# Kernel tuning notes

Hardware: AMD Instinct MI355X
Metric: run time of the kernel (lower is better)

Reference implementation:

```python
import jax, jax.numpy as jnp
import numpy as np
import math

LN_EPS = 1e-5
EPS = 1e-8

def _unfold3(x, stride):
    # torch nn.Unfold(kernel_size=3, stride=stride, padding=1); output [B, C*9, L]
    B, C, H, W = x.shape
    xp = jnp.pad(x, ((0, 0), (0, 0), (1, 1), (1, 1)))
    Ho = (H + 2 - 3) // stride + 1
    Wo = (W + 2 - 3) // stride + 1
    pats = [xp[:, :, i:i + stride * (Ho - 1) + 1:stride, j:j + stride * (Wo - 1) + 1:stride]
            for i in range(3) for j in range(3)]
    out = jnp.stack(pats, axis=2)  # [B,C,9,Ho,Wo]  (c-major, then kh,kw: torch ordering)
    return out.reshape(B, C * 9, Ho * Wo)

def _ln(x, g, b):
    mu = jnp.mean(x, axis=-1, keepdims=True)
    var = jnp.mean((x - mu) ** 2, axis=-1, keepdims=True)
    return (x - mu) * jax.lax.rsqrt(var + LN_EPS) * g + b

def _prm_exp(x, w):
    # x: [B,T,emb], w: [m,emb] -> [B,T,m]
    m = w.shape[0]
    xd = jnp.sum(x * x, axis=-1, keepdims=True) / 2.0
    wtx = jnp.einsum('bte,me->btm', x, w)
    return jnp.exp(wtx - xd) / math.sqrt(m)

def _performer(x, kqv_w, kqv_b, pw, pb, g1, b1, g2, b2, m1w, m1b, m2w, m2b, w):
    # Token_performer.forward (dropout = identity, eval mode)
    h = _ln(x, g1, b1)
    kqv = h @ kqv_w.T + kqv_b
    k, q, v = jnp.split(kqv, 3, axis=-1)  # torch.split order: k, q, v
    kp = _prm_exp(k, w)
    qp = _prm_exp(q, w)
    D = jnp.einsum('btm,bm->bt', qp, kp.sum(axis=1))[..., None]        # [B,T,1]
    kptv = jnp.einsum('btn,btm->bnm', v, kp)                            # [B,emb,m]
    y = jnp.einsum('btm,bnm->btn', qp, kptv) / (D + EPS)                # [B,T,emb]
    y = v + (y @ pw.T + pb)
    h2 = _ln(y, g2, b2)
    mlp = jax.nn.gelu(h2 @ m1w.T + m1b, approximate=False) @ m2w.T + m2b
    return y + mlp

def _forward(x,
             p1_kqv_w, p1_kqv_b, p1_proj_w, p1_proj_b, p1_n1_g, p1_n1_b, p1_n2_g, p1_n2_b,
             p1_m1_w, p1_m1_b, p1_m2_w, p1_m2_b, p1_w,
             p2_kqv_w, p2_kqv_b, p2_proj_w, p2_proj_b, p2_n1_g, p2_n1_b, p2_n2_g, p2_n2_b,
             p2_m1_w, p2_m1_b, p2_m2_w, p2_m2_b, p2_w,
             proj_w, proj_b):
    t = _unfold3(x, 1).transpose(0, 2, 1)  # [B, 50176, 27]
    t = _performer(t, p1_kqv_w, p1_kqv_b, p1_proj_w, p1_proj_b, p1_n1_g, p1_n1_b,
                   p1_n2_g, p1_n2_b, p1_m1_w, p1_m1_b, p1_m2_w, p1_m2_b, p1_w)
    B, N, C = t.shape
    s = int(math.isqrt(N))
    t = t.transpose(0, 2, 1).reshape(B, C, s, s)
    t = _unfold3(t, 2).transpose(0, 2, 1)  # [B, 12544, 576]
    t = _performer(t, p2_kqv_w, p2_kqv_b, p2_proj_w, p2_proj_b, p2_n1_g, p2_n1_b,
                   p2_n2_g, p2_n2_b, p2_m1_w, p2_m1_b, p2_m2_w, p2_m2_b, p2_w)
    B, N, C = t.shape
    s = int(math.isqrt(N))
    t = t.transpose(0, 2, 1).reshape(B, C, s, s)
    t = _unfold3(t, 2).transpose(0, 2, 1)  # [B, 3136, 576]
    return t @ proj_w.T + proj_b           # [B, 3136, 768]

def setup_inputs() -> dict:
    key = jax.random.key(0)
    ks = iter(jax.random.split(key, 40))
    def rn(shape, scale=0.02):
        return (jax.random.normal(next(ks), shape, dtype=jnp.float32) * scale)
    EMB, M = 64, 32
    inp = {'x': jax.random.normal(next(ks), (8, 3, 224, 224), dtype=jnp.float32)}
    for pfx, dim in (('p1', 27), ('p2', 576)):
        inp[f'{pfx}_kqv_w'] = rn((3 * EMB, dim))
        inp[f'{pfx}_kqv_b'] = jnp.zeros((3 * EMB,), jnp.float32)
        inp[f'{pfx}_proj_w'] = rn((EMB, EMB))
        inp[f'{pfx}_proj_b'] = jnp.zeros((EMB,), jnp.float32)
        inp[f'{pfx}_n1_g'] = jnp.ones((dim,), jnp.float32)
        inp[f'{pfx}_n1_b'] = jnp.zeros((dim,), jnp.float32)
        inp[f'{pfx}_n2_g'] = jnp.ones((EMB,), jnp.float32)
        inp[f'{pfx}_n2_b'] = jnp.zeros((EMB,), jnp.float32)
        inp[f'{pfx}_m1_w'] = rn((EMB, EMB))
        inp[f'{pfx}_m1_b'] = jnp.zeros((EMB,), jnp.float32)
        inp[f'{pfx}_m2_w'] = rn((EMB, EMB))
        inp[f'{pfx}_m2_b'] = jnp.zeros((EMB,), jnp.float32)
        # frozen random-feature projection, scaled ~ orthogonal * sqrt(m)
        inp[f'{pfx}_w'] = jax.random.normal(next(ks), (M, EMB), dtype=jnp.float32)
    inp['proj_w'] = rn((768, 576))
    inp['proj_b'] = jnp.zeros((768,), jnp.float32)
    return inp

def reference(x,
              p1_kqv_w, p1_kqv_b, p1_proj_w, p1_proj_b, p1_n1_g, p1_n1_b, p1_n2_g, p1_n2_b,
              p1_m1_w, p1_m1_b, p1_m2_w, p1_m2_b, p1_w,
              p2_kqv_w, p2_kqv_b, p2_proj_w, p2_proj_b, p2_n1_g, p2_n1_b, p2_n2_g, p2_n2_b,
              p2_m1_w, p2_m1_b, p2_m2_w, p2_m2_b, p2_w,
              proj_w, proj_b):
    return _forward(x,
                    p1_kqv_w, p1_kqv_b, p1_proj_w, p1_proj_b, p1_n1_g, p1_n1_b, p1_n2_g, p1_n2_b,
                    p1_m1_w, p1_m1_b, p1_m2_w, p1_m2_b, p1_w,
                    p2_kqv_w, p2_kqv_b, p2_proj_w, p2_proj_b, p2_n1_g, p2_n1_b, p2_n2_g, p2_n2_b,
                    p2_m1_w, p2_m1_b, p2_m2_w, p2_m2_b, p2_w,
                    proj_w, proj_b)
```

## Files before the change

### kernel.cpp

```cpp
#include <hip/hip_runtime.h>
#include <hip/hip_bf16.h>
#include <math.h>

typedef __hip_bfloat16 bf16;
typedef __attribute__((ext_vector_type(8))) short frag8;
typedef __attribute__((ext_vector_type(4))) float f32x4;
typedef long long ll;

__device__ __forceinline__ float b2f(bf16 v) { return __bfloat162float(v); }
__device__ __forceinline__ bf16 f2b(float v) { return __float2bfloat16(v); }

__device__ __forceinline__ unsigned pk2f(float a, float b) {
    union { bf16 h[2]; unsigned u; } c;
    c.h[0] = f2b(a); c.h[1] = f2b(b);
    return c.u;
}
__device__ __forceinline__ void up8(const bf16* p, float* f) {
    const uint4 u = *(const uint4*)p;
    union { unsigned u; bf16 h[2]; } c;
    c.u = u.x; f[0] = b2f(c.h[0]); f[1] = b2f(c.h[1]);
    c.u = u.y; f[2] = b2f(c.h[0]); f[3] = b2f(c.h[1]);
    c.u = u.z; f[4] = b2f(c.h[0]); f[5] = b2f(c.h[1]);
    c.u = u.w; f[6] = b2f(c.h[0]); f[7] = b2f(c.h[1]);
}
__device__ __forceinline__ void up8u(const uint4 u, float* f) {
    union { unsigned u; bf16 h[2]; } c;
    c.u = u.x; f[0] = b2f(c.h[0]); f[1] = b2f(c.h[1]);
    c.u = u.y; f[2] = b2f(c.h[0]); f[3] = b2f(c.h[1]);
    c.u = u.z; f[4] = b2f(c.h[0]); f[5] = b2f(c.h[1]);
    c.u = u.w; f[6] = b2f(c.h[0]); f[7] = b2f(c.h[1]);
}

#define LN_EPS 1e-5f
#define D_EPS 1e-8f
#define INV_SQRT_M 0.17677669529663687f

__global__ __launch_bounds__(256) void k_sniff(const void* x, int* mode)
{
    __shared__ int cnt;
    if (threadIdx.x == 0) cnt = 0;
    __syncthreads();
    const unsigned short* u = (const unsigned short*)x;
    const unsigned short h = u[2 * threadIdx.x];
    const unsigned int bits = ((unsigned int)h) << 16;
    const float v = __uint_as_float(bits);
    const float a = fabsf(v);
    const bool sane = (h == 0) || (a >= 1e-8f && a <= 1e4f);
    if (!sane) atomicAdd(&cnt, 1);
    __syncthreads();
    if (threadIdx.x == 0) *mode = (cnt > 64) ? 1 : 0;
}

struct CvTab { const void* src[28]; int dstOff[28]; int cum[29]; };

__global__ __launch_bounds__(256) void k_convert_all(CvTab tab, bf16* base,
                                                     const int* mode)
{
    const int idx = blockIdx.x * 256 + threadIdx.x;
    if (idx >= tab.cum[28]) return;
    int s = 0;
    while (idx >= tab.cum[s + 1]) ++s;
    const int local = idx - tab.cum[s];
    const float v = (*mode) ? ((const float*)tab.src[s])[local]
                            : b2f(((const bf16*)tab.src[s])[local]);
    base[tab.dstOff[s] + local] = f2b(v);
}

__global__ __launch_bounds__(256) void k_prep(
    const void* __restrict__ w1raw, const int* __restrict__ mode,
    bf16* __restrict__ w1ph, bf16* __restrict__ w1pl)
{
    const int idx = blockIdx.x * 256 + threadIdx.x;
    if (idx >= 6144) return;
    const int o = idx >> 5, k = idx & 31;
    float v = 0.f;
    if (k < 27)
        v = (*mode) ? ((const float*)w1raw)[o * 27 + k]
                    : b2f(((const bf16*)w1raw)[o * 27 + k]);
    const bf16 h = f2b(v);
    w1ph[idx] = h;
    w1pl[idx] = f2b(v - b2f(h));
}

__global__ __launch_bounds__(256) void k_fused1(
    const bf16* __restrict__ x, const bf16* __restrict__ w1ph,
    const bf16* __restrict__ w1pl, const bf16* __restrict__ kqvb,
    const bf16* __restrict__ n1g, const bf16* __restrict__ n1b,
    const bf16* __restrict__ pw,
    bf16* __restrict__ KP, bf16* __restrict__ QP, bf16* __restrict__ V,
    float* __restrict__ red, const int b)
{
    __shared__ __align__(16) char smem[49632];
    bf16 (*wps)[72] = (bf16(*)[72])(smem);
    bf16 (*Ah)[40]  = (bf16(*)[40])(smem + 4608);
    bf16 (*Al)[40]  = (bf16(*)[40])(smem + 9728);
    bf16 (*Th)[72]  = (bf16(*)[72])(smem + 14848);
    bf16 (*Tl)[72]  = (bf16(*)[72])(smem + 24064);
    bf16 (*Wh)[40]  = (bf16(*)[40])(smem + 33280);
    bf16 (*Wl)[40]  = (bf16(*)[40])(smem + 38400);
    bf16 (*KPs)[40] = (bf16(*)[40])(smem + 43520);
    bf16 (*Vs)[72]  = (bf16(*)[72])(smem + 14848);
    float* kbs = (float*)(smem + 48640);
    float* gs  = (float*)(smem + 49408);
    float* bs  = (float*)(smem + 49520);

    const int tid = threadIdx.x;
    {
        const int i = tid * 8;
        *(uint4*)(&wps[i >> 6][i & 63]) = *(const uint4*)(pw + i);
    }
    if (tid < 192) kbs[tid] = b2f(kqvb[tid]);
    if (tid < 27) { gs[tid] = b2f(n1g[tid]); bs[tid] = b2f(n1b[tid]); }
    if (blockIdx.x == 0)
        for (int i = tid; i < 2080; i += 256) red[i] = 0.f;

    const int tok = tid >> 2, part = tid & 3;
    const int t = blockIdx.x * 64 + tok;
    const int h = t / 224, w = t - h * 224;
    const int d0 = part * 7;
    const int nd = (part == 3) ? 6 : 7;
    float vals[7];
    float s = 0.f;
    #pragma unroll
    for (int q = 0; q < 7; ++q) {
        float val = 0.f;
        if (q < nd) {
            const int d = d0 + q;
            const int c = d / 9, rr = d - c * 9;
            const int pi = rr / 3, pj = rr - pi * 3;
            const int hh = h + pi - 1, ww = w + pj - 1;
            if (hh >= 0 && hh < 224 && ww >= 0 && ww < 224)
                val = b2f(x[((ll)(b * 3 + c) * 224 + hh) * 224 + ww]);
        }
        vals[q] = val; s += val;
    }
    s += __shfl_xor(s, 1, 64);  s += __shfl_xor(s, 2, 64);
    const float mean = s * (1.f / 27.f);
    float s2 = 0.f;
    #pragma unroll
    for (int q = 0; q < 7; ++q) {
        if (q < nd) { const float dd = vals[q] - mean; s2 += dd * dd; }
    }
    s2 += __shfl_xor(s2, 1, 64); s2 += __shfl_xor(s2, 2, 64);
    const float rs = rsqrtf(s2 * (1.f / 27.f) + LN_EPS);
    __syncthreads();
    #pragma unroll
    for (int q = 0; q < 7; ++q) {
        if (q < nd) {
            const int d = d0 + q;
            const float nv = (vals[q] - mean) * rs * gs[d] + bs[d];
            const bf16 nh = f2b(nv);
            Ah[tok][d] = nh;
            Al[tok][d] = f2b(nv - b2f(nh));
        }
    }
    if (part == 3) {
        #pragma unroll
        for (int d = 27; d < 32; ++d) { Ah[tok][d] = f2b(0.f); Al[tok][d] = f2b(0.f); }
    }

    const int wv = tid >> 6, lane = tid & 63;
    const int l15 = lane & 15;
    const int k8 = (lane >> 4) << 3;
    const int rbase = (lane >> 4) << 2;
    const int srow = tid >> 2;
    const int scol = (tid & 3) << 3;
    const int colg = (tid & 3) << 4;

    float xdK[4], xdQ[4];

    #pragma unroll
    for (int g = 0; g < 3; ++g) {
        *(uint4*)(&Wh[srow][scol]) = *(const uint4*)(w1ph + (g * 64 + srow) * 32 + scol);
        *(uint4*)(&Wl[srow][scol]) = *(const uint4*)(w1pl + (g * 64 + srow) * 32 + scol);
        __syncthreads();
        const frag8 ah = *(const frag8*)(&Ah[(wv << 4) + l15][k8]);
        const frag8 al = *(const frag8*)(&Al[(wv << 4) + l15][k8]);
        f32x4 acc[4] = {};
        #pragma unroll
        for (int nt = 0; nt < 4; ++nt) {
            const frag8 bh = *(const frag8*)(&Wh[(nt << 4) + l15][k8]);
            const frag8 bl = *(const frag8*)(&Wl[(nt << 4) + l15][k8]);
            acc[nt] = __builtin_amdgcn_mfma_f32_16x16x32_bf16(ah, bh, acc[nt], 0, 0, 0);
            acc[nt] = __builtin_amdgcn_mfma_f32_16x16x32_bf16(al, bh, acc[nt], 0, 0, 0);
            acc[nt] = __builtin_amdgcn_mfma_f32_16x16x32_bf16(ah, bl, acc[nt], 0, 0, 0);
            acc[nt] = __builtin_amdgcn_mfma_f32_16x16x32_bf16(al, bl, acc[nt], 0, 0, 0);
        }
        float xdp[4] = {0.f, 0.f, 0.f, 0.f};
        #pragma unroll
        for (int nt = 0; nt < 4; ++nt) {
            const int col = (nt << 4) + l15;
            const float bv = kbs[g * 64 + col];
            #pragma unroll
            for (int r = 0; r < 4; ++r) {
                const float tb = acc[nt][r] + bv;
                const int trow = (wv << 4) + rbase + r;
                if (g < 2) {
                    const bf16 th = f2b(tb);
                    Th[trow][col] = th;
                    Tl[trow][col] = f2b(tb - b2f(th));
                    xdp[r] += tb * tb;
                } else {
                    Vs[trow][col] = f2b(tb);
                }
            }
        }
        if (g < 2) {
            #pragma unroll
            for (int r = 0; r < 4; ++r) {
                float v = xdp[r];
                v += __shfl_xor(v, 1, 64); v += __shfl_xor(v, 2, 64);
                v += __shfl_xor(v, 4, 64); v += __shfl_xor(v, 8, 64);
                if (g == 0) xdK[r] = 0.5f * v; else xdQ[r] = 0.5f * v;
            }
        }
        __syncthreads();
        if (g < 2) {
            f32x4 acc2[2] = {};
            #pragma unroll
            for (int k0 = 0; k0 < 64; k0 += 32) {
                const frag8 ath = *(const frag8*)(&Th[(wv << 4) + l15][k8 + k0]);
                const frag8 atl = *(const frag8*)(&Tl[(wv << 4) + l15][k8 + k0]);
                #pragma unroll
                for (int nt = 0; nt < 2; ++nt) {
                    const frag8 bw = *(const frag8*)(&wps[(nt << 4) + l15][k8 + k0]);
                    acc2[nt] = __builtin_amdgcn_mfma_f32_16x16x32_bf16(ath, bw, acc2[nt], 0, 0, 0);
                    acc2[nt] = __builtin_amdgcn_mfma_f32_16x16x32_bf16(atl, bw, acc2[nt], 0, 0, 0);
                }
            }
            #pragma unroll
            for (int nt = 0; nt < 2; ++nt)
                #pragma unroll
                for (int r = 0; r < 4; ++r) {
                    const float xd = (g == 0) ? xdK[r] : xdQ[r];
                    const float p = expf(fminf(acc2[nt][r] - xd, 30.f)) * INV_SQRT_M;
                    KPs[(wv << 4) + rbase + r][(nt << 4) + l15] = f2b(p);
                }
            __syncthreads();
            bf16* dstP = (g == 0 ? KP : QP) + ((ll)blockIdx.x * 64 + srow) * 32 + scol;
            *(uint4*)dstP = *(const uint4*)(&KPs[srow][scol]);
            __syncthreads();
        } else {
            bf16* dstV = V + ((ll)blockIdx.x * 64 + srow) * 64 + colg;
            *(uint4*)dstV       = *(const uint4*)(&Vs[srow][colg]);
            *(uint4*)(dstV + 8) = *(const uint4*)(&Vs[srow][colg + 8]);
        }
    }
}

__global__ __launch_bounds__(256) void k_reduce(
    const bf16* __restrict__ kpB, const bf16* __restrict__ vB, const int vstride,
    const int T, float* __restrict__ redBase, const int chunk)
{
    __shared__ bf16 VT[64][72];
    __shared__ bf16 KT[32][72];
    const int bz = blockIdx.y;
    const bf16* kp = kpB + (ll)bz * T * 32;
    const bf16* v  = vB + (ll)bz * T * (ll)vstride;
    float* red = redBase + (ll)bz * 2080;
    const int tid = threadIdx.x;
    const int wv = tid >> 6, lane = tid & 63;
    const int l15 = lane & 15, k8 = (lane >> 4) << 3, rbase = (lane >> 4) << 2;
    const int t0 = blockIdx.x * chunk;

    frag8 ones;
    {
        union { bf16 h; short s; } u; u.h = f2b(1.f);
        #pragma unroll
        for (int i = 0; i < 8; ++i) ones[i] = u.s;
    }

    f32x4 acc[2] = {};
    f32x4 accK[2] = {};

    for (int tt = 0; tt < chunk; tt += 64) {
        const int tb = t0 + tt;
        __syncthreads();
        {
            const int tk = tid >> 2, n0 = (tid & 3) << 4;
            const bf16* src = v + (ll)(tb + tk) * vstride + n0;
            bf16 tmp[16];
            *(uint4*)tmp       = *(const uint4*)src;
            *(uint4*)(tmp + 8) = *(const uint4*)(src + 8);
            #pragma unroll
            for (int j = 0; j < 16; ++j) VT[n0 + j][tk] = tmp[j];
        }
        {
            const int tk = tid >> 2, m0 = (tid & 3) << 3;
            const bf16* src = kp + (ll)(tb + tk) * 32 + m0;
            bf16 tmp[8];
            *(uint4*)tmp = *(const uint4*)src;
            #pragma unroll
            for (int j = 0; j < 8; ++j) KT[m0 + j][tk] = tmp[j];
        }
        __syncthreads();
        #pragma unroll
        for (int ks = 0; ks < 2; ++ks) {
            const frag8 af = *(const frag8*)(&VT[(wv << 4) + l15][k8 + ks * 32]);
            #pragma unroll
            for (int tn = 0; tn < 2; ++tn) {
                const frag8 bfv = *(const frag8*)(&KT[(tn << 4) + l15][k8 + ks * 32]);
                acc[tn] = __builtin_amdgcn_mfma_f32_16x16x32_bf16(af, bfv, acc[tn], 0, 0, 0);
            }
            if (wv == 0) {
                #pragma unroll
                for (int tn = 0; tn < 2; ++tn) {
                    const frag8 bfv = *(const frag8*)(&KT[(tn << 4) + l15][k8 + ks * 32]);
                    accK[tn] = __builtin_amdgcn_mfma_f32_16x16x32_bf16(ones, bfv, accK[tn], 0, 0, 0);
                }
            }
        }
    }
    #pragma unroll
    for (int tn = 0; tn < 2; ++tn) {
        const int m = (tn << 4) + l15;
        #pragma unroll
        for (int r = 0; r < 4; ++r) {
            const int n = (wv << 4) + rbase + r;
            atomicAdd(&red[n * 32 + m], acc[tn][r]);
        }
    }
    if (wv == 0 && (lane >> 4) == 0) {
        #pragma unroll
        for (int tn = 0; tn < 2; ++tn)
            atomicAdd(&red[2048 + (tn << 4) + l15], accK[tn][0]);
    }
}

__global__ __launch_bounds__(256) void k_postmlp(
    const bf16* __restrict__ qpB, const float* __restrict__ redBase,
    const bf16* __restrict__ vB, const int vstride,
    const bf16* __restrict__ pw, const bf16* __restrict__ pb,
    const bf16* __restrict__ n2g, const bf16* __restrict__ n2b,
    const bf16* __restrict__ w1, const bf16* __restrict__ b1,
    const bf16* __restrict__ w2, const bf16* __restrict__ b2,
    bf16* outB, const int T)
{
    __shared__ __align__(16) char smem[47232];
    bf16 (*QPs)[40] = (bf16(*)[40])(smem);
    bf16 (*KH)[40]  = (bf16(*)[40])(smem + 5120);
    bf16 (*KL)[40]  = (bf16(*)[40])(smem + 10240);
    float (*Cs)[72] = (float(*)[72])(smem);
    bf16 (*W1s)[72] = (bf16(*)[72])(smem);
    bf16 (*W2s)[72] = (bf16(*)[72])(smem + 9216);
    bf16 (*PWs)[72] = (bf16(*)[72])(smem + 18432);
    bf16 (*Gs)[72]  = (bf16(*)[72])(smem + 18432);
    bf16 (*Y0H)[72] = (bf16(*)[72])(smem + 27648);
    bf16 (*Ys)[72]  = (bf16(*)[72])(smem + 27648);
    bf16 (*Y0L)[72] = (bf16(*)[72])(smem + 36864);
    bf16 (*Hn)[72]  = (bf16(*)[72])(smem + 36864);
    float* invs  = (float*)(smem + 46080);
    float* pbs   = (float*)(smem + 46336);
    float* ksums = (float*)(smem + 46592);
    float* mns   = (float*)(smem + 46720);
    float* rss   = (float*)(smem + 46976);

    const int tid = threadIdx.x;
    const int bz = blockIdx.y;
    const float* red = redBase + (ll)bz * 2080;
    const bf16* qp = qpB + (ll)bz * (ll)T * 32;
    const bf16* v  = vB + (ll)bz * (ll)T * (ll)vstride;
    bf16* out = outB + (ll)bz * (ll)T * 64;
    const ll m0 = (ll)blockIdx.x * 64;

    const int lr = tid >> 2;
    const int lc8 = (tid & 3) << 3;
    const int lc16 = (tid & 3) << 4;

    *(uint4*)(&QPs[lr][lc8]) = *(const uint4*)(qp + (m0 + lr) * 32 + lc8);
    *(uint4*)(&PWs[lr][lc16])     = *(const uint4*)(pw + lr * 64 + lc16);
    *(uint4*)(&PWs[lr][lc16 + 8]) = *(const uint4*)(pw + lr * 64 + lc16 + 8);
    {
        const int i0 = tid * 8;
        const float4 a = *(const float4*)(red + i0);
        const float4 b = *(const float4*)(red + i0 + 4);
        const int n = i0 >> 5, m = i0 & 31;
        float xs[8] = {a.x, a.y, a.z, a.w, b.x, b.y, b.z, b.w};
        #pragma unroll
        for (int k = 0; k < 8; ++k) {
            const bf16 h = f2b(xs[k]);
            KH[n][m + k] = h;
            KL[n][m + k] = f2b(xs[k] - b2f(h));
        }
    }
    if (tid < 32) ksums[tid] = red[2048 + tid];
    if (tid < 64) pbs[tid] = b2f(pb[tid]);
    __syncthreads();

    if (tid < 64) {
        float D = D_EPS;
        #pragma unroll
        for (int m = 0; m < 32; ++m) D += b2f(QPs[tid][m]) * ksums[m];
        invs[tid] = 1.f / D;
    }

    const int wv = tid >> 6, lane = tid & 63;
    const int l15 = lane & 15;
    const int mr = (wv << 4) + l15;
    const int k8 = (lane >> 4) << 3;
    const int rbase = (lane >> 4) << 2;

    f32x4 acc[4] = {};
    {
        const frag8 af = *(const frag8*)(&QPs[mr][k8]);
        #pragma unroll
        for (int tn = 0; tn < 4; ++tn) {
            const int nr = (tn << 4) + l15;
            const frag8 bh = *(const frag8*)(&KH[nr][k8]);
            acc[tn] = __builtin_amdgcn_mfma_f32_16x16x32_bf16(af, bh, acc[tn], 0, 0, 0);
            const frag8 bl = *(const frag8*)(&KL[nr][k8]);
            acc[tn] = __builtin_amdgcn_mfma_f32_16x16x32_bf16(af, bl, acc[tn], 0, 0, 0);
        }
    }
    #pragma unroll
    for (int tn = 0; tn < 4; ++tn) {
        const int n = (tn << 4) + l15;
        #pragma unroll
        for (int r = 0; r < 4; ++r) {
            const float x = acc[tn][r];
            const bf16 h = f2b(x);
            Y0H[(wv << 4) + rbase + r][n] = h;
            Y0L[(wv << 4) + rbase + r][n] = f2b(x - b2f(h));
        }
    }
    __syncthreads();

    f32x4 acc2[4] = {};
    #pragma unroll
    for (int k0 = 0; k0 < 64; k0 += 32) {
        const frag8 ah = *(const frag8*)(&Y0H[mr][k8 + k0]);
        const frag8 al = *(const frag8*)(&Y0L[mr][k8 + k0]);
        #pragma unroll
        for (int tn = 0; tn < 4; ++tn) {
            const frag8 bw = *(const frag8*)(&PWs[(tn << 4) + l15][k8 + k0]);
            acc2[tn] = __builtin_amdgcn_mfma_f32_16x16x32_bf16(ah, bw, acc2[tn], 0, 0, 0);
            acc2[tn] = __builtin_amdgcn_mfma_f32_16x16x32_bf16(al, bw, acc2[tn], 0, 0, 0);
        }
    }
    #pragma unroll
    for (int tn = 0; tn < 4; ++tn) {
        const int n = (tn << 4) + l15;
        #pragma unroll
        for (int r = 0; r < 4; ++r) {
            const int row = (wv << 4) + rbase + r;
            Cs[row][n] = acc2[tn][r] * invs[row] + pbs[n];
        }
    }
    __syncthreads();

    {
        const int row = tid >> 2;
        const bf16* vsrc = v + (m0 + row) * (ll)vstride + lc16;
        #pragma unroll
        for (int hh = 0; hh < 2; ++hh) {
            float vv[8];
            up8(vsrc + hh * 8, vv);
            const float* cp = &Cs[row][lc16 + hh * 8];
            uint4 st;
            st.x = pk2f(cp[0] + vv[0], cp[1] + vv[1]);
            st.y = pk2f(cp[2] + vv[2], cp[3] + vv[3]);
            st.z = pk2f(cp[4] + vv[4], cp[5] + vv[5]);
            st.w = pk2f(cp[6] + vv[6], cp[7] + vv[7]);
            *(uint4*)(&Ys[row][lc16 + hh * 8]) = st;
        }
    }
    __syncthreads();

    if (tid < 64) {
        float s = 0.f, s2 = 0.f;
        #pragma unroll
        for (int n = 0; n < 64; ++n) { const float vv = b2f(Ys[tid][n]); s += vv; s2 += vv * vv; }
        const float mn = s * (1.f / 64.f);
        const float var = fmaxf(s2 * (1.f / 64.f) - mn * mn, 0.f);
        mns[tid] = mn; rss[tid] = rsqrtf(var + LN_EPS);
    }
    *(uint4*)(&W1s[lr][lc16])     = *(const uint4*)(w1 + lr * 64 + lc16);
    *(uint4*)(&W1s[lr][lc16 + 8]) = *(const uint4*)(w1 + lr * 64 + lc16 + 8);
    *(uint4*)(&W2s[lr][lc16])     = *(const uint4*)(w2 + lr * 64 + lc16);
    *(uint4*)(&W2s[lr][lc16 + 8]) = *(const uint4*)(w2 + lr * 64 + lc16 + 8);
    __syncthreads();

    for (int i = tid; i < 4096; i += 256) {
        const int r = i >> 6, c = i & 63;
        Hn[r][c] = f2b((b2f(Ys[r][c]) - mns[r]) * rss[r] * b2f(n2g[c]) + b2f(n2b[c]));
    }
    __syncthreads();

    f32x4 accm[4] = {};
    #pragma unroll
    for (int k0 = 0; k0 < 64; k0 += 32) {
        const frag8 af = *(const frag8*)(&Hn[mr][k8 + k0]);
        #pragma unroll
        for (int tn = 0; tn < 4; ++tn) {
            const frag8 bfv = *(const frag8*)(&W1s[(tn << 4) + l15][k8 + k0]);
            accm[tn] = __builtin_amdgcn_mfma_f32_16x16x32_bf16(af, bfv, accm[tn], 0, 0, 0);
        }
    }
    #pragma unroll
    for (int tn = 0; tn < 4; ++tn) {
        const int n = (tn << 4) + l15;
        const float bv = b2f(b1[n]);
        #pragma unroll
        for (int r = 0; r < 4; ++r) {
            float vg = accm[tn][r] + bv;
            vg = 0.5f * vg * (1.f + erff(vg * 0.70710678118654752f));
            Gs[(wv << 4) + rbase + r][n] = f2b(vg);
        }
    }
    __syncthreads();

    f32x4 accn[4] = {};
    #pragma unroll
    for (int k0 = 0; k0 < 64; k0 += 32) {
        const frag8 af = *(const frag8*)(&Gs[mr][k8 + k0]);
        #pragma unroll
        for (int tn = 0; tn < 4; ++tn) {
            const frag8 bfv = *(const frag8*)(&W2s[(tn << 4) + l15][k8 + k0]);
            accn[tn] = __builtin_amdgcn_mfma_f32_16x16x32_bf16(af, bfv, accn[tn], 0, 0, 0);
        }
    }
    #pragma unroll
    for (int tn = 0; tn < 4; ++tn) {
        const int n = (tn << 4) + l15;
        const float bv = b2f(b2[n]);
        #pragma unroll
        for (int r = 0; r < 4; ++r)
            Hn[(wv << 4) + rbase + r][n] = f2b(accn[tn][r] + bv);
    }
    __syncthreads();

    {
        const int row = tid >> 2;
        bf16* dst = out + (m0 + row) * 64 + lc16;
        #pragma unroll
        for (int hh = 0; hh < 2; ++hh) {
            float sv[8], rv[8];
            up8(&Hn[row][lc16 + hh * 8], sv);
            up8(&Ys[row][lc16 + hh * 8], rv);
            uint4 st;
            st.x = pk2f(sv[0] + rv[0], sv[1] + rv[1]);
            st.y = pk2f(sv[2] + rv[2], sv[3] + rv[3]);
            st.z = pk2f(sv[4] + rv[4], sv[5] + rv[5]);
            st.w = pk2f(sv[6] + rv[6], sv[7] + rv[7]);
            *(uint4*)(dst + hh * 8) = st;
        }
    }
}

__global__ __launch_bounds__(256) void k_unfold576(
    const bf16* __restrict__ in, const int Hin, const int Ho,
    const bf16* __restrict__ g, const bf16* __restrict__ bb,
    const int do_ln, bf16* __restrict__ A,
    const ll inBStride, const ll outBStride)
{
    in += (ll)blockIdx.y * inBStride;
    A  += (ll)blockIdx.y * outBStride;
    const int t = blockIdx.x * 4 + (threadIdx.x >> 6);
    const int l = threadIdx.x & 63;
    const int ho = t / Ho, wo = t - ho * Ho;
    float vals[9];
    float s = 0.f;
    #pragma unroll
    for (int r = 0; r < 9; ++r) {
        const int d = l + (r << 6);
        const int c = d / 9;
        const int rr = d - c * 9;
        const int i = rr / 3, j = rr - i * 3;
        const int hh = 2 * ho + i - 1, ww = 2 * wo + j - 1;
        float val = 0.f;
        if (hh >= 0 && hh < Hin && ww >= 0 && ww < Hin)
            val = b2f(in[((ll)hh * Hin + ww) * 64 + c]);
        vals[r] = val; s += val;
    }
    bf16* out = A + (ll)t * 576;
    if (do_ln) {
        #pragma unroll
        for (int o = 32; o > 0; o >>= 1) s += __shfl_xor(s, o, 64);
        const float mean = s * (1.f / 576.f);
        float s2 = 0.f;
        #pragma unroll
        for (int r = 0; r < 9; ++r) { const float dd = vals[r] - mean; s2 += dd * dd; }
        #pragma unroll
        for (int o = 32; o > 0; o >>= 1) s2 += __shfl_xor(s2, o, 64);
        const float rs = rsqrtf(s2 * (1.f / 576.f) + LN_EPS);
        #pragma unroll
        for (int r = 0; r < 9; ++r) {
            const int d = l + (r << 6);
            out[d] = f2b((vals[r] - mean) * rs * b2f(g[d]) + b2f(bb[d]));
        }
    } else {
        #pragma unroll
        for (int r = 0; r < 9; ++r) out[l + (r << 6)] = f2b(vals[r]);
    }
}

__global__ __launch_bounds__(256) void k_gemm(
    const bf16* __restrict__ A, const int lda,
    const bf16* __restrict__ W,
    const bf16* __restrict__ bias,
    const bf16* res, const int ldres,
    void* C, const int ldc, const ll mOff,
    const int K, const int* outm)
{
    __shared__ bf16 As[2][64][40];
    __shared__ bf16 Bs[2][64][40];
    __shared__ bf16 Cs[64][72];
    const int tid = threadIdx.x;
    const int wv = tid >> 6;
    const int lane = tid & 63;
    const ll m0 = (ll)blockIdx.x * 64;
    const int n0 = blockIdx.y * 64;
    f32x4 acc[4] = {};
    const int lr = tid >> 2;
    const int lc = (tid & 3) << 3;
    const int mr = (wv << 4) + (lane & 15);
    const int k8 = (lane >> 4) << 3;
    const bf16* Ag = A + (m0 + lr) * (ll)lda + lc;
    const bf16* Wg = W + (ll)(n0 + lr) * K + lc;

    uint4 av  = *(const uint4*)(Ag);
    uint4 wv4 = *(const uint4*)(Wg);
    *(uint4*)(&As[0][lr][lc]) = av;
    *(uint4*)(&Bs[0][lr][lc]) = wv4;
    int cur = 0;
    __syncthreads();
    for (int k0 = 0; k0 < K; k0 += 32) {
        const bool nxt = (k0 + 32 < K);
        if (nxt) {
            av  = *(const uint4*)(Ag + k0 + 32);
            wv4 = *(const uint4*)(Wg + k0 + 32);
        }
        const frag8 af = *(const frag8*)(&As[cur][mr][k8]);
        #pragma unroll
        for (int tn = 0; tn < 4; ++tn) {
            const frag8 bfv = *(const frag8*)(&Bs[cur][(tn << 4) + (lane & 15)][k8]);
            acc[tn] = __builtin_amdgcn_mfma_f32_16x16x32_bf16(af, bfv, acc[tn], 0, 0, 0);
        }
        if (nxt) {
            *(uint4*)(&As[cur ^ 1][lr][lc]) = av;
            *(uint4*)(&Bs[cur ^ 1][lr][lc]) = wv4;
        }
        __syncthreads();
        cur ^= 1;
    }
    const int om = outm ? *outm : 0;
    const int rbase = (lane >> 4) << 2;
    if (om) {
        #pragma unroll
        for (int tn = 0; tn < 4; ++tn) {
            const int n = n0 + (tn << 4) + (lane & 15);
            const float bv = bias ? b2f(bias[n]) : 0.f;
            #pragma unroll
            for (int r = 0; r < 4; ++r) {
                const ll m = m0 + (wv << 4) + rbase + r;
                float v = acc[tn][r] + bv;
                if (res) v += b2f(res[m * (ll)ldres + n]);
                ((float*)C)[(m + mOff) * (ll)ldc + n] = v;
            }
        }
        return;
    }
    #pragma unroll
    for (int tn = 0; tn < 4; ++tn) {
        const int nl = (tn << 4) + (lane & 15);
        const float bv = bias ? b2f(bias[n0 + nl]) : 0.f;
        #pragma unroll
        for (int r = 0; r < 4; ++r) {
            const ll m = m0 + (wv << 4) + rbase + r;
            float v = acc[tn][r] + bv;
            if (res) v += b2f(res[m * (ll)ldres + n0 + nl]);
            Cs[(wv << 4) + rbase + r][nl] = f2b(v);
        }
    }
    __syncthreads();
    const int row = tid >> 2;
    const int colg = (tid & 3) << 4;
    bf16* dst = (bf16*)C + (m0 + mOff + row) * (ll)ldc + n0 + colg;
    *(uint4*)dst       = *(const uint4*)(&Cs[row][colg]);
    *(uint4*)(dst + 8) = *(const uint4*)(&Cs[row][colg + 8]);
}

__global__ __launch_bounds__(256) void k_fusedP2(
    const bf16* __restrict__ kqv, const bf16* __restrict__ pw,
    bf16* __restrict__ KP, bf16* __restrict__ QP,
    float* __restrict__ redBase, const int T)
{
    __shared__ __align__(16) char smem[19200];
    bf16 (*Ks)[72]  = (bf16(*)[72])(smem);
    bf16 (*wps)[72] = (bf16(*)[72])(smem + 9216);
    bf16 (*KPs)[40] = (bf16(*)[40])(smem + 13824);
    float* xds = (float*)(smem + 18944);

    const int tid = threadIdx.x;
    const int bz = blockIdx.y;
    {
        const int i = tid * 8;
        *(uint4*)(&wps[i >> 6][i & 63]) = *(const uint4*)(pw + i);
    }
    if (blockIdx.x == 0) {
        float* red = redBase + (ll)bz * 2080;
        for (int i = tid; i < 2080; i += 256) red[i] = 0.f;
    }
    const ll gt0 = (ll)bz * T + (ll)blockIdx.x * 64;
    const int srow = tid >> 2;
    const int colg = (tid & 3) << 4;
    const int scol = (tid & 3) << 3;
    const int wv = tid >> 6, lane = tid & 63;
    const int l15 = lane & 15, k8 = (lane >> 4) << 3, rbase = (lane >> 4) << 2;

    #pragma unroll
    for (int p = 0; p < 2; ++p) {
        const bf16* src = kqv + (gt0 + srow) * 192 + p * 64 + colg;
        const uint4 u0 = *(const uint4*)src;
        const uint4 u1 = *(const uint4*)(src + 8);
        *(uint4*)(&Ks[srow][colg])     = u0;
        *(uint4*)(&Ks[srow][colg + 8]) = u1;
        float f0[8], f1[8];
        up8u(u0, f0); up8u(u1, f1);
        float s2 = 0.f;
        #pragma unroll
        for (int k = 0; k < 8; ++k) s2 += f0[k] * f0[k] + f1[k] * f1[k];
        s2 += __shfl_xor(s2, 1, 64); s2 += __shfl_xor(s2, 2, 64);
        if ((tid & 3) == 0) xds[srow] = 0.5f * s2;
        __syncthreads();
        f32x4 acc2[2] = {};
        #pragma unroll
        for (int k0 = 0; k0 < 64; k0 += 32) {
            const frag8 af = *(const frag8*)(&Ks[(wv << 4) + l15][k8 + k0]);
            #pragma unroll
            for (int nt = 0; nt < 2; ++nt) {
                const frag8 bw = *(const frag8*)(&wps[(nt << 4) + l15][k8 + k0]);
                acc2[nt] = __builtin_amdgcn_mfma_f32_16x16x32_bf16(af, bw, acc2[nt], 0, 0, 0);
            }
        }
        #pragma unroll
        for (int nt = 0; nt < 2; ++nt)
            #pragma unroll
            for (int r = 0; r < 4; ++r) {
                const int trow = (wv << 4) + rbase + r;
                const float pv = expf(fminf(acc2[nt][r] - xds[trow], 30.f)) * INV_SQRT_M;
                KPs[trow][(nt << 4) + l15] = f2b(pv);
            }
        __syncthreads();
        bf16* dst = (p == 0 ? KP : QP) + (gt0 + srow) * 32 + scol;
        *(uint4*)dst = *(const uint4*)(&KPs[srow][scol]);
        __syncthreads();
    }
}

extern "C" void kernel_launch(void* const* d_in, const int* in_sizes, int n_in,
                              void* d_out, int out_size, void* d_ws, size_t ws_size,
                              hipStream_t stream)
{
    (void)in_sizes; (void)n_in; (void)out_size;
    const int T1 = 50176, T2 = 12544;
    char* ws = (char*)d_ws;

    size_t cur = 0;
    auto alloc = [&](size_t bytes) {
        size_t r = cur; cur += (bytes + 127) & ~(size_t)127; return r;
    };
    static const int segIdx[28] = {0, 2, 3, 4, 5, 6, 7, 8, 9, 10, 11, 12, 13,
                                   14, 15, 16, 17, 18, 19, 20, 21, 22, 23, 24, 25, 26, 27, 28};
    static const int segN[28] = {1204224, 192, 4096, 64, 27, 27, 64, 64, 4096, 64, 4096, 64, 2048,
                                 110592, 192, 4096, 64, 576, 576, 64, 64, 4096, 64, 4096, 64, 2048,
                                 442368, 768};
    size_t segOff[28];
    for (int i = 0; i < 28; ++i) segOff[i] = alloc((size_t)segN[i] * 2);
    const size_t oMODE = alloc(256);
    const size_t oRED  = alloc(66560);
    const size_t oW1P  = alloc(24576);
    const size_t oBIG  = alloc(6422528);
    const size_t oKP   = alloc(3211264);
    const size_t oQP   = alloc(3211264);
    (void)oQP;

    bf16* P[28];
    for (int i = 0; i < 28; ++i) P[i] = (bf16*)(ws + segOff[i]);
    bf16* XC = P[0];
    bf16 *P1KQVB = P[1], *P1PW = P[2], *P1PB = P[3], *P1N1G = P[4], *P1N1B = P[5];
    bf16 *P1N2G = P[6], *P1N2B = P[7], *P1M1W = P[8], *P1M1B = P[9], *P1M2W = P[10];
    bf16 *P1M2B = P[11], *P1W = P[12];
    bf16 *P2KQVW = P[13], *P2KQVB = P[14], *P2PW = P[15], *P2PB = P[16];
    bf16 *P2N1G = P[17], *P2N1B = P[18], *P2N2G = P[19], *P2N2B = P[20];
    bf16 *P2M1W = P[21], *P2M1B = P[22], *P2M2W = P[23], *P2M2B = P[24], *P2W = P[25];
    bf16 *PROJW = P[26], *PROJB = P[27];

    int*   MODE = (int*)(ws + oMODE);
    float* REDF = (float*)(ws + oRED);
    bf16*  W1PH = (bf16*)(ws + oW1P);
    bf16*  W1PL = (bf16*)(ws + oW1P + 12288);
    bf16*  BIG  = (bf16*)(ws + oBIG);
    bf16*  KP   = (bf16*)(ws + oKP);
    bf16*  QP   = (bf16*)(ws + oKP + 3211264);
    bf16*  A2   = (bf16*)(ws + oKP);
    bf16*  KQV2F = (bf16*)d_out;
    bf16*  KP2F  = (bf16*)(ws + oKP);
    bf16*  QP2F  = (bf16*)(ws + oKP + 6422528);
    bf16*  YB2F  = (bf16*)(ws + oBIG);
    bf16*  A3c   = (bf16*)(ws + oBIG + 12845056);

    k_sniff<<<1, 256, 0, stream>>>(d_in[0], MODE);
    CvTab tab;
    int cum = 0;
    for (int i = 0; i < 28; ++i) {
        tab.src[i] = d_in[segIdx[i]];
        tab.dstOff[i] = (int)(segOff[i] / 2);
        tab.cum[i] = cum;
        cum += segN[i];
    }
    tab.cum[28] = cum;
    k_convert_all<<<(cum + 255) / 256, 256, 0, stream>>>(tab, (bf16*)ws, MODE);
    k_prep<<<24, 256, 0, stream>>>(d_in[1], MODE, W1PH, W1PL);

    for (int b = 0; b < 8; ++b) {
        float* REDb = REDF + (ll)b * 2080;
        k_fused1<<<784, 256, 0, stream>>>(XC, W1PH, W1PL, P1KQVB, P1N1G, P1N1B,
                                          P1W, KP, QP, BIG, REDb, b);
        k_reduce<<<dim3(392, 1), 256, 0, stream>>>(KP, BIG, 64, T1, REDb, 128);
        k_postmlp<<<dim3(784, 1), 256, 0, stream>>>(QP, REDb, BIG, 64, P1PW, P1PB,
            P1N2G, P1N2B, P1M1W, P1M1B, P1M2W, P1M2B, BIG, T1);
        k_unfold576<<<dim3(3136, 1), 256, 0, stream>>>(BIG, 224, 112, P2N1G, P2N1B,
                                                       1, A2, 0, 0);
        k_gemm<<<dim3(196, 3), 256, 0, stream>>>(A2, 576, P2KQVW, P2KQVB,
            nullptr, 0, KQV2F, 192, (ll)b * T2, 576, nullptr);
    }

    k_fusedP2<<<dim3(196, 8), 256, 0, stream>>>(KQV2F, P2W, KP2F, QP2F, REDF, T2);
    k_reduce<<<dim3(98, 8), 256, 0, stream>>>(KP2F, KQV2F + 128, 192, T2, REDF, 128);
    k_postmlp<<<dim3(196, 8), 256, 0, stream>>>(QP2F, REDF, KQV2F + 128, 192,
        P2PW, P2PB, P2N2G, P2N2B, P2M1W, P2M1B, P2M2W, P2M2B, YB2F, T2);

    const size_t needFull = oBIG + 12845056 + (size_t)25088 * 576 * 2;
    if (ws_size >= needFull) {
        bf16* A3 = (bf16*)(ws + oBIG + 12845056);
        k_unfold576<<<dim3(784, 8), 256, 0, stream>>>(
            YB2F, 112, 56, nullptr, nullptr, 0, A3, (ll)T2 * 64, (ll)3136 * 576);
        k_gemm<<<dim3(392, 12), 256, 0, stream>>>(A3, 576, PROJW, PROJB,
            nullptr, 0, d_out, 768, 0, 576, MODE);
    } else {
        for (int c = 0; c < 4; ++c) {
            k_unfold576<<<dim3(784, 2), 256, 0, stream>>>(
                YB2F + (ll)(2 * c) * T2 * 64, 112, 56, nullptr, nullptr, 0,
                A3c, (ll)T2 * 64, (ll)3136 * 576);
            k_gemm<<<dim3(98, 12), 256, 0, stream>>>(A3c, 576, PROJW, PROJB,
                nullptr, 0, d_out, 768, (ll)c * 6272, 576, MODE);
        }
    }
}
```

Baseline: 974.0 us.

## Remap GEMM blocks XCD-aware with N-fastest order and stage fp32 epilogue via LDS

Changes the k_gemm launch to a 1D grid and remaps block IDs so consecutive tiles land on the same XCD, with N tiles varying fastest. This lets blocks that share an A row-tile hit the same L2. The fp32 output path now stages results in a shared buffer and writes them as coalesced 16-byte vectors, replacing scattered scalar stores. This adds an extra barrier and a larger LDS footprint, which can reduce occupancy.

New measurement: 1.012 ms. 3.9% more time.

```diff
diff --git a/kernel.cpp b/kernel.cpp
--- a/kernel.cpp
+++ b/kernel.cpp
@@ -600,16 +600,28 @@
     const bf16* __restrict__ bias,
     const bf16* res, const int ldres,
     void* C, const int ldc, const ll mOff,
-    const int K, const int* outm)
+    const int K, const int* outm, const int gridN)
 {
     __shared__ bf16 As[2][64][40];
     __shared__ bf16 Bs[2][64][40];
-    __shared__ bf16 Cs[64][72];
+    __shared__ __align__(16) char epi[17408];
+    float (*Cf)[68] = (float(*)[68])epi;
+    bf16 (*Cs)[72] = (bf16(*)[72])epi;
+
+    const int nwg = gridDim.x;
+    const int orig = blockIdx.x;
+    const int xcd = orig & 7;
+    const int q = nwg >> 3, r = nwg & 7;
+    const int wgid = (xcd < r ? xcd * (q + 1) : r * (q + 1) + (xcd - r) * q)
+                     + (orig >> 3);
+    const int mTile = wgid / gridN;
+    const int nTile = wgid - mTile * gridN;
+    const ll m0 = (ll)mTile * 64;
+    const int n0 = nTile * 64;
+
     const int tid = threadIdx.x;
     const int wv = tid >> 6;
     const int lane = tid & 63;
-    const ll m0 = (ll)blockIdx.x * 64;
-    const int n0 = blockIdx.y * 64;
     f32x4 acc[4] = {};
     const int lr = tid >> 2;
     const int lc = (tid & 3) << 3;
@@ -648,16 +660,23 @@
     if (om) {
         #pragma unroll
         for (int tn = 0; tn < 4; ++tn) {
-            const int n = n0 + (tn << 4) + (lane & 15);
-            const float bv = bias ? b2f(bias[n]) : 0.f;
+            const int nl = (tn << 4) + (lane & 15);
+            const float bv = bias ? b2f(bias[n0 + nl]) : 0.f;
             #pragma unroll
             for (int r = 0; r < 4; ++r) {
                 const ll m = m0 + (wv << 4) + rbase + r;
                 float v = acc[tn][r] + bv;
-                if (res) v += b2f(res[m * (ll)ldres + n]);
-                ((float*)C)[(m + mOff) * (ll)ldc + n] = v;
+                if (res) v += b2f(res[m * (ll)ldres + n0 + nl]);
+                Cf[(wv << 4) + rbase + r][nl] = v;
             }
         }
+        __syncthreads();
+        const int row = tid >> 2;
+        const int cg = (tid & 3) << 4;
+        float* dst = (float*)C + (m0 + mOff + row) * (ll)ldc + n0 + cg;
+        #pragma unroll
+        for (int u = 0; u < 4; ++u)
+            *(uint4*)(dst + u * 4) = *(const uint4*)(&Cf[row][cg + u * 4]);
         return;
     }
     #pragma unroll
@@ -822,8 +841,8 @@
             P1N2G, P1N2B, P1M1W, P1M1B, P1M2W, P1M2B, BIG, T1);
         k_unfold576<<<dim3(3136, 1), 256, 0, stream>>>(BIG, 224, 112, P2N1G, P2N1B,
                                                        1, A2, 0, 0);
-        k_gemm<<<dim3(196, 3), 256, 0, stream>>>(A2, 576, P2KQVW, P2KQVB,
-            nullptr, 0, KQV2F, 192, (ll)b * T2, 576, nullptr);
+        k_gemm<<<588, 256, 0, stream>>>(A2, 576, P2KQVW, P2KQVB,
+            nullptr, 0, KQV2F, 192, (ll)b * T2, 576, nullptr, 3);
     }
 
     k_fusedP2<<<dim3(196, 8), 256, 0, stream>>>(KQV2F, P2W, KP2F, QP2F, REDF, T2);
@@ -836,15 +855,15 @@
         bf16* A3 = (bf16*)(ws + oBIG + 12845056);
         k_unfold576<<<dim3(784, 8), 256, 0, stream>>>(
             YB2F, 112, 56, nullptr, nullptr, 0, A3, (ll)T2 * 64, (ll)3136 * 576);
-        k_gemm<<<dim3(392, 12), 256, 0, stream>>>(A3, 576, PROJW, PROJB,
-            nullptr, 0, d_out, 768, 0, 576, MODE);
+        k_gemm<<<4704, 256, 0, stream>>>(A3, 576, PROJW, PROJB,
+            nullptr, 0, d_out, 768, 0, 576, MODE, 12);
     } else {
         for (int c = 0; c < 4; ++c) {
             k_unfold576<<<dim3(784, 2), 256, 0, stream>>>(
                 YB2F + (ll)(2 * c) * T2 * 64, 112, 56, nullptr, nullptr, 0,
                 A3c, (ll)T2 * 64, (ll)3136 * 576);
-            k_gemm<<<dim3(98, 12), 256, 0, stream>>>(A3c, 576, PROJW, PROJB,
-                nullptr, 0, d_out, 768, (ll)c * 6272, 576, MODE);
-        }
-    }
-}
+            k_gemm<<<1176, 256, 0, stream>>>(A3c, 576, PROJW, PROJB,
+                nullptr, 0, d_out, 768, (ll)c * 6272, 576, MODE, 12);
+        }
+    }
+}
```

## Add 128x128 double-buffered MFMA GEMM with XCD-aware tile mapping for final projection

Applied to the files above, without the earlier changes.

Adds a new GEMM kernel for the final 576->768 projection. It uses 128x128 output tiles with double-buffered LDS and register prefetch of the next K slice, and remaps workgroup IDs so neighbouring tiles land on the same XCD. The larger tiles raise MFMA work per byte loaded and cut redundant A/W reads compared with the old 64-wide GEMM. In exchange the kernel uses more registers and LDS, which can lower occupancy, and the grid is smaller.

Result: no change. 963.6 us (median of 2 runs) (-1.1%).

```diff
diff --git a/kernel.cpp b/kernel.cpp
--- a/kernel.cpp
+++ b/kernel.cpp
@@ -680,6 +680,109 @@
     *(uint4*)(dst + 8) = *(const uint4*)(&Cs[row][colg + 8]);
 }
 
+__global__ __launch_bounds__(256) void k_gemm128(
+    const bf16* __restrict__ A, const int lda,
+    const bf16* __restrict__ W,
+    const bf16* __restrict__ bias,
+    void* C, const int ldc, const ll mOff,
+    const int K, const int* outm, const int gridN)
+{
+    __shared__ __align__(16) char smem[40960];
+    bf16 (*As)[128][40] = (bf16(*)[128][40])smem;
+    bf16 (*Bs)[128][40] = (bf16(*)[128][40])(smem + 20480);
+    bf16 (*Cs)[136]     = (bf16(*)[136])smem;
+
+    const int nwg = gridDim.x;
+    const int orig = blockIdx.x;
+    const int xcd = orig & 7;
+    const int q = nwg >> 3, r = nwg & 7;
+    const int wgid = (xcd < r ? xcd * (q + 1) : r * (q + 1) + (xcd - r) * q)
+                     + (orig >> 3);
+    const int mTile = wgid / gridN;
+    const int nTile = wgid - mTile * gridN;
+    const ll m0 = (ll)mTile * 128;
+    const int n0 = nTile * 128;
+
+    const int tid = threadIdx.x;
+    const int wv = tid >> 6, lane = tid & 63, l15 = lane & 15;
+    const int k8 = (lane >> 4) << 3;
+    const int rbase = (lane >> 4) << 2;
+    const int mr0 = (wv << 5) + l15;
+    const int sr = tid >> 1, sc = (tid & 1) << 4;
+    const bf16* Ag = A + (m0 + sr) * (ll)lda + sc;
+    const bf16* Wg = W + (ll)(n0 + sr) * K + sc;
+
+    f32x4 acc[2][8] = {};
+    uint4 a0 = *(const uint4*)(Ag);
+    uint4 a1 = *(const uint4*)(Ag + 8);
+    uint4 b0 = *(const uint4*)(Wg);
+    uint4 b1 = *(const uint4*)(Wg + 8);
+    *(uint4*)(&(*As)[sr][sc])     = a0;
+    *(uint4*)(&(*As)[sr][sc + 8]) = a1;
+    *(uint4*)(&(*Bs)[sr][sc])     = b0;
+    *(uint4*)(&(*Bs)[sr][sc + 8]) = b1;
+    int cur = 0;
+    __syncthreads();
+    for (int k0 = 0; k0 < K; k0 += 32) {
+        const bool nxt = (k0 + 32 < K);
+        if (nxt) {
+            a0 = *(const uint4*)(Ag + k0 + 32);
+            a1 = *(const uint4*)(Ag + k0 + 40);
+            b0 = *(const uint4*)(Wg + k0 + 32);
+            b1 = *(const uint4*)(Wg + k0 + 40);
+        }
+        const frag8 af0 = *(const frag8*)(&As[cur][mr0][k8]);
+        const frag8 af1 = *(const frag8*)(&As[cur][mr0 + 16][k8]);
+        #pragma unroll
+        for (int tn = 0; tn < 8; ++tn) {
+            const frag8 bfv = *(const frag8*)(&Bs[cur][(tn << 4) + l15][k8]);
+            acc[0][tn] = __builtin_amdgcn_mfma_f32_16x16x32_bf16(af0, bfv, acc[0][tn], 0, 0, 0);
+            acc[1][tn] = __builtin_amdgcn_mfma_f32_16x16x32_bf16(af1, bfv, acc[1][tn], 0, 0, 0);
+        }
+        if (nxt) {
+            *(uint4*)(&As[cur ^ 1][sr][sc])     = a0;
+            *(uint4*)(&As[cur ^ 1][sr][sc + 8]) = a1;
+            *(uint4*)(&Bs[cur ^ 1][sr][sc])     = b0;
+            *(uint4*)(&Bs[cur ^ 1][sr][sc + 8]) = b1;
+        }
+        __syncthreads();
+        cur ^= 1;
+    }
+    const int om = outm ? *outm : 0;
+    if (om) {
+        #pragma unroll
+        for (int mi = 0; mi < 2; ++mi)
+            #pragma unroll
+            for (int tn = 0; tn < 8; ++tn) {
+                const int n = n0 + (tn << 4) + l15;
+                const float bv = bias ? b2f(bias[n]) : 0.f;
+                #pragma unroll
+                for (int rr2 = 0; rr2 < 4; ++rr2) {
+                    const ll m = m0 + (wv << 5) + (mi << 4) + rbase + rr2;
+                    ((float*)C)[(m + mOff) * (ll)ldc + n] = acc[mi][tn][rr2] + bv;
+                }
+            }
+        return;
+    }
+    #pragma unroll
+    for (int mi = 0; mi < 2; ++mi)
+        #pragma unroll
+        for (int tn = 0; tn < 8; ++tn) {
+            const int nl = (tn << 4) + l15;
+            const float bv = bias ? b2f(bias[n0 + nl]) : 0.f;
+            #pragma unroll
+            for (int rr2 = 0; rr2 < 4; ++rr2)
+                Cs[(wv << 5) + (mi << 4) + rbase + rr2][nl] = f2b(acc[mi][tn][rr2] + bv);
+        }
+    __syncthreads();
+    const int row = tid >> 1;
+    const int colg = (tid & 1) << 6;
+    bf16* dst = (bf16*)C + (m0 + mOff + row) * (ll)ldc + n0 + colg;
+    #pragma unroll
+    for (int u = 0; u < 8; ++u)
+        *(uint4*)(dst + u * 8) = *(const uint4*)(&Cs[row][colg + u * 8]);
+}
+
 __global__ __launch_bounds__(256) void k_fusedP2(
     const bf16* __restrict__ kqv, const bf16* __restrict__ pw,
     bf16* __restrict__ KP, bf16* __restrict__ QP,
@@ -836,15 +939,15 @@
         bf16* A3 = (bf16*)(ws + oBIG + 12845056);
         k_unfold576<<<dim3(784, 8), 256, 0, stream>>>(
             YB2F, 112, 56, nullptr, nullptr, 0, A3, (ll)T2 * 64, (ll)3136 * 576);
-        k_gemm<<<dim3(392, 12), 256, 0, stream>>>(A3, 576, PROJW, PROJB,
-            nullptr, 0, d_out, 768, 0, 576, MODE);
+        k_gemm128<<<1176, 256, 0, stream>>>(A3, 576, PROJW, PROJB,
+            d_out, 768, 0, 576, MODE, 6);
     } else {
         for (int c = 0; c < 4; ++c) {
             k_unfold576<<<dim3(784, 2), 256, 0, stream>>>(
                 YB2F + (ll)(2 * c) * T2 * 64, 112, 56, nullptr, nullptr, 0,
                 A3c, (ll)T2 * 64, (ll)3136 * 576);
-            k_gemm<<<dim3(98, 12), 256, 0, stream>>>(A3c, 576, PROJW, PROJB,
-                nullptr, 0, d_out, 768, (ll)c * 6272, 576, MODE);
-        }
-    }
-}
+            k_gemm128<<<294, 256, 0, stream>>>(A3c, 576, PROJW, PROJB,
+                d_out, 768, (ll)c * 6272, 576, MODE, 6);
+        }
+    }
+}
```
